# Performance work log

Hardware: AMD Instinct MI355X
Metric: run time of the kernel (lower is better)

The kernel has to match this reference:

```python
import jax, jax.numpy as jnp
import numpy as np

N_HEADS = 32
N_KV_HEADS = 8
HEAD_DIM = 128
DIM = 4096
ROPE_THETA = 500000.0
BSZ, SEQLEN = 4, 1024


def _rope(t, cos, sin):
    # t: [B,S,H,hd]; cos/sin: [S,hd//2]
    te = t[..., 0::2]
    to = t[..., 1::2]
    c = cos[None, :, None, :]
    s = sin[None, :, None, :]
    out = jnp.stack([te * c - to * s, te * s + to * c], axis=-1)
    return out.reshape(t.shape)


def setup_inputs() -> dict:
    key = jax.random.key(0)
    ks = jax.random.split(key, 8)
    scale = 1.0 / np.sqrt(DIM)
    x = jax.random.normal(ks[0], (BSZ, SEQLEN, DIM), dtype=jnp.float32)
    wq = jax.random.normal(ks[1], (DIM, N_HEADS * HEAD_DIM), dtype=jnp.float32) * scale
    wk = jax.random.normal(ks[2], (DIM, N_KV_HEADS * HEAD_DIM), dtype=jnp.float32) * scale
    wv = jax.random.normal(ks[3], (DIM, N_KV_HEADS * HEAD_DIM), dtype=jnp.float32) * scale
    wo = jax.random.normal(ks[4], (N_HEADS * HEAD_DIM, DIM), dtype=jnp.float32) * scale
    # rotary tables: freqs_cis[s, j] = exp(i * s * theta^(-2j/hd))
    inv_freq = 1.0 / (ROPE_THETA ** (np.arange(0, HEAD_DIM, 2, dtype=np.float32) / HEAD_DIM))
    ang = np.outer(np.arange(SEQLEN, dtype=np.float32), inv_freq)
    freqs_cos = jnp.asarray(np.cos(ang), dtype=jnp.float32)
    freqs_sin = jnp.asarray(np.sin(ang), dtype=jnp.float32)
    # additive causal mask: 0 on/below diag, -inf above
    causal_mask = jnp.triu(jnp.full((SEQLEN, SEQLEN), -jnp.inf, dtype=jnp.float32), k=1)
    return {"x": x, "wq": wq, "wk": wk, "wv": wv, "wo": wo,
            "freqs_cos": freqs_cos, "freqs_sin": freqs_sin,
            "causal_mask": causal_mask, "fixed_point_iter": 0, "start_pos": 0}


def reference(x, wq, wk, wv, wo, freqs_cos, freqs_sin, causal_mask, fixed_point_iter, start_pos):
    B, S, _ = x.shape
    n_rep = N_HEADS // N_KV_HEADS
    xq = (x @ wq).reshape(B, S, N_HEADS, HEAD_DIM)
    xk = (x @ wk).reshape(B, S, N_KV_HEADS, HEAD_DIM)
    xv = (x @ wv).reshape(B, S, N_KV_HEADS, HEAD_DIM)
    xq = _rope(xq, freqs_cos, freqs_sin)
    xk = _rope(xk, freqs_cos, freqs_sin)
    # start_pos == 0 prefill: cache slice [:start_pos+S] equals freshly written xk/xv
    keys = jnp.repeat(xk, n_rep, axis=2)    # [B,S,H,hd]
    values = jnp.repeat(xv, n_rep, axis=2)
    scores = jnp.einsum('bqhd,bkhd->bhqk', xq, keys) / np.sqrt(HEAD_DIM)
    scores = scores + causal_mask  # broadcast [S,S]
    probs = jax.nn.softmax(scores.astype(jnp.float32), axis=-1).astype(xq.dtype)
    out = jnp.einsum('bhqk,bkhd->bqhd', probs, values)
    out = out.reshape(B, S, N_HEADS * HEAD_DIM)
    return out @ wo
```

## Files before the change

### kernel.cpp

```cpp
#include <hip/hip_runtime.h>

#define BSZ_  4
#define SEQ_  1024
#define NH_   32
#define NKVH_ 8
#define HD_   128
#define DIM_  4096
#define NTOK_ (BSZ_ * SEQ_)
#define QKVW_ 6144

typedef float  floatx4  __attribute__((ext_vector_type(4)));
typedef float  floatx16 __attribute__((ext_vector_type(16)));
typedef __bf16 bf16x8   __attribute__((ext_vector_type(8)));
typedef unsigned short ushortx8 __attribute__((ext_vector_type(8)));
typedef unsigned int   uint4v   __attribute__((ext_vector_type(4)));

__device__ __forceinline__ float fast_exp2(float x) {
  return __builtin_amdgcn_exp2f(x);
}

__device__ __forceinline__ unsigned short f2bf_bits(float f) {
  unsigned int u = __float_as_uint(f);
  u += 0x7FFFu + ((u >> 16) & 1u);
  return (unsigned short)(u >> 16);
}
__device__ __forceinline__ unsigned int pack_bf2_rne(float lo, float hi_) {
  return (unsigned int)f2bf_bits(lo) | ((unsigned int)f2bf_bits(hi_) << 16);
}
__device__ __forceinline__ unsigned int pack_bf2_trunc(float lo, float hi_) {
  return __builtin_amdgcn_perm(__float_as_uint(hi_), __float_as_uint(lo), 0x07060302u);
}

__device__ __forceinline__ void gld16(const void* g, void* l) {
  __builtin_amdgcn_global_load_lds(
      (const __attribute__((address_space(1))) void*)g,
      (__attribute__((address_space(3))) void*)l, 16, 0, 0);
}

__global__ __launch_bounds__(256)
void xconv(const float* __restrict__ X, unsigned short* __restrict__ XB)
{
  size_t i = ((size_t)blockIdx.x * 256 + threadIdx.x) * 4;
  float4 v = *(const float4*)&X[i];
  ushort4 o;
  o.x = f2bf_bits(v.x); o.y = f2bf_bits(v.y);
  o.z = f2bf_bits(v.z); o.w = f2bf_bits(v.w);
  *(ushort4*)&XB[i] = o;
}

__global__ __launch_bounds__(256)
void wtrans(const float* __restrict__ W, unsigned short* __restrict__ WT,
            int K, int N)
{
  __shared__ unsigned short T[32][36];
  const int k0 = blockIdx.y * 32, n0 = blockIdx.x * 32;
  const int t = threadIdx.x;
  {
    int kr = t >> 3, nc = (t & 7) * 4;
    float4 v = *(const float4*)&W[(size_t)(k0 + kr) * N + n0 + nc];
    T[kr][nc + 0] = f2bf_bits(v.x);
    T[kr][nc + 1] = f2bf_bits(v.y);
    T[kr][nc + 2] = f2bf_bits(v.z);
    T[kr][nc + 3] = f2bf_bits(v.w);
  }
  __syncthreads();
  {
    int nr = t >> 3, kc = (t & 7) * 4;
    ushort4 o;
    o.x = T[kc + 0][nr]; o.y = T[kc + 1][nr];
    o.z = T[kc + 2][nr]; o.w = T[kc + 3][nr];
    *(ushort4*)&WT[(size_t)(n0 + nr) * K + k0 + kc] = o;
  }
}

__global__ __launch_bounds__(256)
void vtrans2(const unsigned short* __restrict__ qkv, unsigned short* __restrict__ VT)
{
  __shared__ unsigned short T[32][36];
  const int bh = blockIdx.z;
  const int s0 = blockIdx.x * 32, d0 = blockIdx.y * 32;
  const int b = bh >> 3, kvh = bh & 7;
  const int t = threadIdx.x;
  {
    int sr = t >> 3, dc = (t & 7) * 4;
    ushort4 v = *(const ushort4*)&qkv[(size_t)(b * SEQ_ + s0 + sr) * QKVW_ + 5120 + kvh * HD_ + d0 + dc];
    T[sr][dc + 0] = v.x; T[sr][dc + 1] = v.y;
    T[sr][dc + 2] = v.z; T[sr][dc + 3] = v.w;
  }
  __syncthreads();
  {
    int dr = t >> 3, sc = (t & 7) * 4;
    ushort4 o;
    o.x = T[sc + 0][dr]; o.y = T[sc + 1][dr];
    o.z = T[sc + 2][dr]; o.w = T[sc + 3][dr];
    *(ushort4*)&VT[((size_t)bh * HD_ + d0 + dr) * SEQ_ + s0 + sc] = o;
  }
}

__global__ __launch_bounds__(256)
void rope2(unsigned int* __restrict__ t, const float* __restrict__ cosf,
           const float* __restrict__ sinf, int shift, int stride_u32, int base_u32)
{
  int idx = blockIdx.x * 256 + threadIdx.x;
  int tok = idx >> shift;
  int rem = idx & ((1 << shift) - 1);
  int d2  = idx & 63;
  int pos = tok & (SEQ_ - 1);
  unsigned int* p = &t[(size_t)tok * stride_u32 + base_u32 + rem];
  unsigned int pv = *p;
  float xe = __uint_as_float(pv << 16);
  float xo = __uint_as_float(pv & 0xFFFF0000u);
  float cv = cosf[pos * 64 + d2];
  float sv = sinf[pos * 64 + d2];
  float oe = xe * cv - xo * sv;
  float oo = xe * sv + xo * cv;
  *p = pack_bf2_rne(oe, oo);
}

template<bool OUT_BF16>
__global__ __launch_bounds__(1024, 4)
void gemm_w16(const unsigned short* __restrict__ A,
              const unsigned short* __restrict__ B,
              void* __restrict__ Cout, int M, int N, int K)
{
  __shared__ __align__(16) unsigned short As[4][256][32];
  __shared__ __align__(16) unsigned short Bs[4][256][32];

  const int tid  = threadIdx.x;
  const int w    = tid >> 6;
  const int lane = tid & 63;
  const int l16  = lane & 15;
  const int quad = lane >> 4;
  const int wr   = w >> 2;
  const int wc   = w & 3;

  int wg = blockIdx.x;
  const int q8 = gridDim.x >> 3;
  wg = (wg & 7) * q8 + (wg >> 3);
  const int nbx = N >> 8;
  const int bm = (wg / nbx) * 256;
  const int bn = (wg % nbx) * 256;

  const int srow = tid >> 2;
  const int scs  = (tid & 3) ^ ((srow >> 1) & 3);
  const unsigned short* Ag = &A[(size_t)(bm + srow) * K + scs * 8];
  const unsigned short* Bg = &B[(size_t)(bn + srow) * K + scs * 8];
  char* AsW = (char*)&As[0][0][0] + w * 1024;
  char* BsW = (char*)&Bs[0][0][0] + w * 1024;

  const int ntiles = K >> 5;

  auto stage = [&](int kt, int buf) {
    size_t ko = (size_t)kt << 5;
    gld16(Ag + ko, AsW + buf * 16384);
    gld16(Bg + ko, BsW + buf * 16384);
  };

  floatx4 acc[4][4];
#pragma unroll
  for (int i = 0; i < 4; i++)
#pragma unroll
    for (int j = 0; j < 4; j++) acc[i][j] = (floatx4){0.f, 0.f, 0.f, 0.f};

  const int cfr = quad ^ ((l16 >> 1) & 3);
  const unsigned short* ArF = &As[0][wr * 64][cfr * 8];
  const unsigned short* BrF = &Bs[0][wc * 64][cfr * 8];

  stage(0, 0); stage(1, 1); stage(2, 2);
  asm volatile("s_waitcnt vmcnt(4)" ::: "memory");
  __builtin_amdgcn_s_barrier();

#pragma unroll 1
  for (int t = 0; t < ntiles; t++) {
    const int buf = t & 3;

    bf16x8 af[4], bfr[4];
    {
      const unsigned short* Ab = ArF + (size_t)buf * (256 * 32) + l16 * 32;
      const unsigned short* Bb = BrF + (size_t)buf * (256 * 32) + l16 * 32;
#pragma unroll
      for (int i = 0; i < 4; i++) af[i]  = *(const bf16x8*)&Ab[i * (16 * 32)];
#pragma unroll
      for (int j = 0; j < 4; j++) bfr[j] = *(const bf16x8*)&Bb[j * (16 * 32)];
    }

    {
      int pk = (t + 3 < ntiles) ? t + 3 : 0;
      stage(pk, (t + 3) & 3);
    }

    __builtin_amdgcn_s_setprio(1);
#pragma unroll
    for (int i = 0; i < 4; i++)
#pragma unroll
      for (int j = 0; j < 4; j++)
        acc[i][j] = __builtin_amdgcn_mfma_f32_16x16x32_bf16(af[i], bfr[j], acc[i][j], 0, 0, 0);
    __builtin_amdgcn_s_setprio(0);

    asm volatile("s_waitcnt vmcnt(4)" ::: "memory");
    __builtin_amdgcn_s_barrier();
  }

  asm volatile("s_waitcnt vmcnt(0)" ::: "memory");

#pragma unroll
  for (int i = 0; i < 4; i++)
#pragma unroll
    for (int j = 0; j < 4; j++)
#pragma unroll
      for (int r = 0; r < 4; r++) {
        size_t row = bm + wr * 64 + i * 16 + quad * 4 + r;
        size_t col = bn + wc * 64 + j * 16 + l16;
        if (OUT_BF16)
          ((unsigned short*)Cout)[row * N + col] = f2bf_bits(acc[i][j][r]);
        else
          ((float*)Cout)[row * N + col] = acc[i][j][r];
      }
}

__global__ __launch_bounds__(256, 2)
void flash_attn2(const unsigned short* __restrict__ qkv,
                 const unsigned short* __restrict__ vt,
                 unsigned short* __restrict__ o)
{
  __shared__ __align__(16) unsigned short S_[4][8192];
  unsigned short* Ks = &S_[0][0];
  unsigned short* Vs = &S_[1][0];

  const int bid = blockIdx.x;
  const int grp = bid >> 7;
  const int idx = bid & 127;
  const int qt = (grp == 0) ? 3 : (grp == 1) ? 2 : (grp == 2) ? 0 : 1;
  const int h = idx & 31, b = idx >> 5;

  const int kvh = h >> 2;
  const int tid = threadIdx.x, w = tid >> 6, lane = tid & 63;
  const int l31 = lane & 31, hi = lane >> 5;
  const int qb = qt * 256, qw = qb + w * 64;

  const float CEXP = (float)(0.08838834764831845 * 1.4426950408889634);

  bf16x8 qf[2][8];
#pragma unroll
  for (int t2 = 0; t2 < 2; t2++) {
    const unsigned short* qrow =
        &qkv[(size_t)(b * SEQ_ + qw + t2 * 32 + l31) * QKVW_ + h * HD_ + hi * 8];
#pragma unroll
    for (int s = 0; s < 8; s++)
      qf[t2][s] = *(const bf16x8*)&qrow[s * 16];
  }

  floatx16 oa[2][4];
#pragma unroll
  for (int t2 = 0; t2 < 2; t2++)
#pragma unroll
    for (int dt = 0; dt < 4; dt++)
#pragma unroll
      for (int r = 0; r < 16; r++) oa[t2][dt][r] = 0.f;

  float ms[2] = {-3.0e38f, -3.0e38f};
  float ls[2] = {0.f, 0.f};

  const int nk = qb + 256;
  const int qmaxw = qw + 63;

  ushortx8 kreg[4], vreg[4];
  const size_t kg0 = (size_t)(b * SEQ_) * QKVW_ + 4096 + kvh * HD_;
  const size_t vg0 = ((size_t)(b * NKVH_ + kvh) * HD_) * SEQ_;
  const int krow = tid >> 4, kc = tid & 15;
  const int vrow = tid >> 3, vc = tid & 7;

  auto issue_loads = [&](int kb) {
    const size_t gb = kg0 + (size_t)kb * QKVW_;
#pragma unroll
    for (int it = 0; it < 4; it++)
      kreg[it] = *(const ushortx8*)&qkv[gb + (size_t)(it * 16 + krow) * QKVW_ + kc * 8];
    const size_t vb = vg0 + kb;
#pragma unroll
    for (int it = 0; it < 4; it++)
      vreg[it] = *(const ushortx8*)&vt[vb + (size_t)(it * 32 + vrow) * SEQ_ + vc * 8];
  };
  auto write_lds = [&]() {
#pragma unroll
    for (int it = 0; it < 4; it++) {
      int key = it * 16 + krow;
      *(ushortx8*)&Ks[key * 128 + ((kc ^ (key & 15)) * 8)] = kreg[it];
    }
#pragma unroll
    for (int it = 0; it < 4; it++) {
      int d = it * 32 + vrow;
      *(ushortx8*)&Vs[d * 64 + ((vc ^ (d & 7)) * 8)] = vreg[it];
    }
  };

  issue_loads(0);

  for (int kb_ = 0; kb_ < nk; kb_ += 64) {
    __syncthreads();
    write_lds();
    if (kb_ + 64 < nk) issue_loads(kb_ + 64);
    asm volatile("s_waitcnt lgkmcnt(0)" ::: "memory");
    __builtin_amdgcn_s_barrier();

    if (kb_ <= qmaxw) {
      const bool needmask = (kb_ + 63 > qw);

#pragma unroll
      for (int t2 = 0; t2 < 2; t2++) {
        floatx16 sc[2];
#pragma unroll
        for (int r = 0; r < 16; r++) { sc[0][r] = 0.f; sc[1][r] = 0.f; }
        __builtin_amdgcn_s_setprio(1);
#pragma unroll
        for (int s = 0; s < 8; s++) {
          int c = 2 * s + hi;
          bf16x8 k0 = *(const bf16x8*)&Ks[l31 * 128 + ((c ^ (l31 & 15)) * 8)];
          bf16x8 k1 = *(const bf16x8*)&Ks[(32 + l31) * 128 + ((c ^ ((32 + l31) & 15)) * 8)];
          sc[0] = __builtin_amdgcn_mfma_f32_32x32x16_bf16(k0, qf[t2][s], sc[0], 0, 0, 0);
          sc[1] = __builtin_amdgcn_mfma_f32_32x32x16_bf16(k1, qf[t2][s], sc[1], 0, 0, 0);
        }
        __builtin_amdgcn_s_setprio(0);

        if (needmask) {
          const int q = qw + t2 * 32 + l31;
#pragma unroll
          for (int k2 = 0; k2 < 2; k2++)
#pragma unroll
            for (int r = 0; r < 16; r++) {
              int key = kb_ + k2 * 32 + (r & 3) + 8 * (r >> 2) + 4 * hi;
              if (key > q) sc[k2][r] = -3.0e38f;
            }
        }

        float mx0 = sc[0][0], mx1 = sc[0][1];
#pragma unroll
        for (int r = 2; r < 16; r += 2) { mx0 = fmaxf(mx0, sc[0][r]); mx1 = fmaxf(mx1, sc[0][r + 1]); }
#pragma unroll
        for (int r = 0; r < 16; r += 2) { mx0 = fmaxf(mx0, sc[1][r]); mx1 = fmaxf(mx1, sc[1][r + 1]); }
        float mx = fmaxf(mx0, mx1);
        mx = fmaxf(mx, __shfl_xor(mx, 32));
        float mxs = mx * CEXP;

        float mn, alpha;
        if (__all(mxs - ms[t2] <= 8.0f)) {
          mn = ms[t2]; alpha = 1.0f;
        } else {
          mn = fmaxf(ms[t2], mxs);
          alpha = fast_exp2(ms[t2] - mn);
          ms[t2] = mn;
        }

        float rs0 = 0.f, rs1 = 0.f;
        unsigned int pk2[2][8];
#pragma unroll
        for (int k2 = 0; k2 < 2; k2++) {
#pragma unroll
          for (int r = 0; r < 16; r += 2) {
            float p0 = fast_exp2(__builtin_fmaf(sc[k2][r],     CEXP, -mn));
            float p1 = fast_exp2(__builtin_fmaf(sc[k2][r + 1], CEXP, -mn));
            rs0 += p0; rs1 += p1;
            pk2[k2][r >> 1] = pack_bf2_trunc(p0, p1);
          }
        }
        float rs = rs0 + rs1;
        rs += __shfl_xor(rs, 32);
        ls[t2] = ls[t2] * alpha + rs;

        if (__any(alpha != 1.0f)) {
#pragma unroll
          for (int dt = 0; dt < 4; dt++)
#pragma unroll
            for (int r = 0; r < 16; r++) oa[t2][dt][r] *= alpha;
        }

        __builtin_amdgcn_s_setprio(1);
#pragma unroll
        for (int ks = 0; ks < 4; ks++) {
          const int k2s = ks >> 1;
          const int sub = (ks & 1) * 4;
          auto w02 = __builtin_amdgcn_permlane32_swap(pk2[k2s][sub + 0], pk2[k2s][sub + 2], false, false);
          auto w13 = __builtin_amdgcn_permlane32_swap(pk2[k2s][sub + 1], pk2[k2s][sub + 3], false, false);
          uint4v pw = (uint4v){(unsigned int)w02[0], (unsigned int)w13[0],
                               (unsigned int)w02[1], (unsigned int)w13[1]};
          bf16x8 pf = __builtin_bit_cast(bf16x8, pw);
          int c = 2 * ks + hi;
#pragma unroll
          for (int dt = 0; dt < 4; dt++) {
            int d = dt * 32 + l31;
            bf16x8 vf = *(const bf16x8*)&Vs[d * 64 + ((c ^ (d & 7)) * 8)];
            oa[t2][dt] = __builtin_amdgcn_mfma_f32_32x32x16_bf16(vf, pf, oa[t2][dt], 0, 0, 0);
          }
        }
        __builtin_amdgcn_s_setprio(0);
      }
    }
  }

  __syncthreads();
  unsigned short* patch = &S_[w][0];
  float inv[2] = {1.0f / ls[0], 1.0f / ls[1]};
#pragma unroll
  for (int t2 = 0; t2 < 2; t2++) {
    const int qloc = t2 * 32 + l31;
#pragma unroll
    for (int dt = 0; dt < 4; dt++)
#pragma unroll
      for (int rq = 0; rq < 4; rq++) {
        float a0 = oa[t2][dt][rq * 4 + 0] * inv[t2];
        float a1 = oa[t2][dt][rq * 4 + 1] * inv[t2];
        float a2 = oa[t2][dt][rq * 4 + 2] * inv[t2];
        float a3 = oa[t2][dt][rq * 4 + 3] * inv[t2];
        int doff = dt * 32 + 8 * rq + 4 * hi;
        int c = doff >> 3;
        uint2 val = {pack_bf2_rne(a0, a1), pack_bf2_rne(a2, a3)};
        *(uint2*)&patch[qloc * 128 + ((c ^ (qloc & 7)) * 8) + (doff & 7)] = val;
      }
  }
#pragma unroll
  for (int it = 0; it < 16; it++) {
    int idx2 = it * 64 + lane;
    int row = idx2 >> 4, c = idx2 & 15;
    int cc = (c & 7) ^ (row & 7);
    int cs = (c & 8) | cc;
    ushortx8 vv = *(const ushortx8*)&patch[row * 128 + cs * 8];
    *(ushortx8*)&o[(size_t)(b * SEQ_ + qb + w * 64 + row) * 4096 + h * HD_ + c * 8] = vv;
  }
}

extern "C" void kernel_launch(void* const* d_in, const int* in_sizes, int n_in,
                              void* d_out, int out_size, void* d_ws, size_t ws_size,
                              hipStream_t stream)
{
  const float* x  = (const float*)d_in[0];
  const float* wq = (const float*)d_in[1];
  const float* wk = (const float*)d_in[2];
  const float* wv = (const float*)d_in[3];
  const float* wo = (const float*)d_in[4];
  const float* fc = (const float*)d_in[5];
  const float* fs = (const float*)d_in[6];
  float* out = (float*)d_out;

  unsigned short* xb    = (unsigned short*)d_ws;
  unsigned short* wqkvT = xb    + (size_t)NTOK_ * DIM_;
  unsigned short* qkvb  = wqkvT + (size_t)QKVW_ * DIM_;
  unsigned short* vtb   = qkvb  + (size_t)NTOK_ * QKVW_;
  unsigned short* ab    = xb;
  unsigned short* woT   = wqkvT;

  dim3 blk(256);

  xconv<<<(NTOK_ * DIM_ / 4) / 256, blk, 0, stream>>>(x, xb);
  wtrans<<<dim3(DIM_ / 32, DIM_ / 32), blk, 0, stream>>>(wq, wqkvT, DIM_, DIM_);
  wtrans<<<dim3((NKVH_ * HD_) / 32, DIM_ / 32), blk, 0, stream>>>(wk, wqkvT + (size_t)4096 * DIM_, DIM_, NKVH_ * HD_);
  wtrans<<<dim3((NKVH_ * HD_) / 32, DIM_ / 32), blk, 0, stream>>>(wv, wqkvT + (size_t)5120 * DIM_, DIM_, NKVH_ * HD_);

  gemm_w16<true><<<dim3((QKVW_ / 256) * (NTOK_ / 256)), dim3(1024), 0, stream>>>(
      xb, wqkvT, qkvb, NTOK_, QKVW_, DIM_);

  wtrans<<<dim3(DIM_ / 32, DIM_ / 32), blk, 0, stream>>>(wo, woT, DIM_, DIM_);

  rope2<<<(NTOK_ * 2048) / 256, blk, 0, stream>>>((unsigned int*)qkvb, fc, fs, 11, 3072, 0);
  rope2<<<(NTOK_ * 512) / 256, blk, 0, stream>>>((unsigned int*)qkvb, fc, fs, 9, 3072, 2048);

  vtrans2<<<dim3(SEQ_ / 32, HD_ / 32, BSZ_ * NKVH_), blk, 0, stream>>>(qkvb, vtb);

  flash_attn2<<<dim3((SEQ_ / 256) * NH_ * BSZ_), blk, 0, stream>>>(qkvb, vtb, ab);

  gemm_w16<false><<<dim3((DIM_ / 256) * (NTOK_ / 256)), dim3(1024), 0, stream>>>(
      ab, woT, out, NTOK_, DIM_, DIM_);
}
```

Measured before the change: 677.8 us.

## Merge weight transposes and rope launches, batch PV MFMAs across query tiles

Combines the three Q/K/V weight-transpose launches into one kernel and the two rope launches into one, cutting launch overhead and tail effects. In flash attention, the P·V MFMA loop is moved out of the per-query-tile loop so each V fragment read from LDS feeds two MFMAs, one per query tile. This halves V LDS reads and interleaves independent MFMA chains. In exchange, the packed probabilities of both tiles stay live at once, which raises register pressure.

```diff
diff --git a/kernel.cpp b/kernel.cpp
--- a/kernel.cpp
+++ b/kernel.cpp
@@ -46,6 +46,36 @@
   o.x = f2bf_bits(v.x); o.y = f2bf_bits(v.y);
   o.z = f2bf_bits(v.z); o.w = f2bf_bits(v.w);
   *(ushort4*)&XB[i] = o;
+}
+
+__global__ __launch_bounds__(256)
+void wtrans3(const float* __restrict__ wq, const float* __restrict__ wk,
+             const float* __restrict__ wv, unsigned short* __restrict__ WT)
+{
+  __shared__ unsigned short T[32][36];
+  const int n0 = blockIdx.x * 32;
+  const int k0 = blockIdx.y * 32;
+  const float* W; int ns0, Nsrc;
+  if (n0 < 4096)      { W = wq; ns0 = n0;        Nsrc = 4096; }
+  else if (n0 < 5120) { W = wk; ns0 = n0 - 4096; Nsrc = 1024; }
+  else                { W = wv; ns0 = n0 - 5120; Nsrc = 1024; }
+  const int t = threadIdx.x;
+  {
+    int kr = t >> 3, nc = (t & 7) * 4;
+    float4 v = *(const float4*)&W[(size_t)(k0 + kr) * Nsrc + ns0 + nc];
+    T[kr][nc + 0] = f2bf_bits(v.x);
+    T[kr][nc + 1] = f2bf_bits(v.y);
+    T[kr][nc + 2] = f2bf_bits(v.z);
+    T[kr][nc + 3] = f2bf_bits(v.w);
+  }
+  __syncthreads();
+  {
+    int nr = t >> 3, kc = (t & 7) * 4;
+    ushort4 o;
+    o.x = T[kc + 0][nr]; o.y = T[kc + 1][nr];
+    o.z = T[kc + 2][nr]; o.w = T[kc + 3][nr];
+    *(ushort4*)&WT[(size_t)(n0 + nr) * DIM_ + k0 + kc] = o;
+  }
 }
 
 __global__ __launch_bounds__(256)
@@ -98,15 +128,17 @@
 }
 
 __global__ __launch_bounds__(256)
-void rope2(unsigned int* __restrict__ t, const float* __restrict__ cosf,
-           const float* __restrict__ sinf, int shift, int stride_u32, int base_u32)
+void rope_all(unsigned int* __restrict__ t, const float* __restrict__ cosf,
+              const float* __restrict__ sinf)
 {
   int idx = blockIdx.x * 256 + threadIdx.x;
-  int tok = idx >> shift;
-  int rem = idx & ((1 << shift) - 1);
-  int d2  = idx & 63;
+  const int NQ = NTOK_ * 2048;
+  int tok, rem, base;
+  if (idx < NQ) { tok = idx >> 11; rem = idx & 2047; base = 0; }
+  else { int j = idx - NQ; tok = j >> 9; rem = j & 511; base = 2048; }
+  int d2  = rem & 63;
   int pos = tok & (SEQ_ - 1);
-  unsigned int* p = &t[(size_t)tok * stride_u32 + base_u32 + rem];
+  unsigned int* p = &t[(size_t)tok * 3072 + base + rem];
   unsigned int pv = *p;
   float xe = __uint_as_float(pv << 16);
   float xo = __uint_as_float(pv & 0xFFFF0000u);
@@ -304,6 +336,7 @@
 
     if (kb_ <= qmaxw) {
       const bool needmask = (kb_ + 63 > qw);
+      unsigned int pkt[2][2][8];
 
 #pragma unroll
       for (int t2 = 0; t2 < 2; t2++) {
@@ -351,7 +384,6 @@
         }
 
         float rs0 = 0.f, rs1 = 0.f;
-        unsigned int pk2[2][8];
 #pragma unroll
         for (int k2 = 0; k2 < 2; k2++) {
 #pragma unroll
@@ -359,7 +391,7 @@
             float p0 = fast_exp2(__builtin_fmaf(sc[k2][r],     CEXP, -mn));
             float p1 = fast_exp2(__builtin_fmaf(sc[k2][r + 1], CEXP, -mn));
             rs0 += p0; rs1 += p1;
-            pk2[k2][r >> 1] = pack_bf2_trunc(p0, p1);
+            pkt[t2][k2][r >> 1] = pack_bf2_trunc(p0, p1);
           }
         }
         float rs = rs0 + rs1;
@@ -372,27 +404,38 @@
 #pragma unroll
             for (int r = 0; r < 16; r++) oa[t2][dt][r] *= alpha;
         }
-
-        __builtin_amdgcn_s_setprio(1);
-#pragma unroll
-        for (int ks = 0; ks < 4; ks++) {
-          const int k2s = ks >> 1;
-          const int sub = (ks & 1) * 4;
-          auto w02 = __builtin_amdgcn_permlane32_swap(pk2[k2s][sub + 0], pk2[k2s][sub + 2], false, false);
-          auto w13 = __builtin_amdgcn_permlane32_swap(pk2[k2s][sub + 1], pk2[k2s][sub + 3], false, false);
+      }
+
+      __builtin_amdgcn_s_setprio(1);
+#pragma unroll
+      for (int ks = 0; ks < 4; ks++) {
+        const int k2s = ks >> 1;
+        const int sub = (ks & 1) * 4;
+        bf16x8 pf0, pf1;
+        {
+          auto w02 = __builtin_amdgcn_permlane32_swap(pkt[0][k2s][sub + 0], pkt[0][k2s][sub + 2], false, false);
+          auto w13 = __builtin_amdgcn_permlane32_swap(pkt[0][k2s][sub + 1], pkt[0][k2s][sub + 3], false, false);
           uint4v pw = (uint4v){(unsigned int)w02[0], (unsigned int)w13[0],
                                (unsigned int)w02[1], (unsigned int)w13[1]};
-          bf16x8 pf = __builtin_bit_cast(bf16x8, pw);
-          int c = 2 * ks + hi;
-#pragma unroll
-          for (int dt = 0; dt < 4; dt++) {
-            int d = dt * 32 + l31;
-            bf16x8 vf = *(const bf16x8*)&Vs[d * 64 + ((c ^ (d & 7)) * 8)];
-            oa[t2][dt] = __builtin_amdgcn_mfma_f32_32x32x16_bf16(vf, pf, oa[t2][dt], 0, 0, 0);
-          }
-        }
-        __builtin_amdgcn_s_setprio(0);
+          pf0 = __builtin_bit_cast(bf16x8, pw);
+        }
+        {
+          auto w02 = __builtin_amdgcn_permlane32_swap(pkt[1][k2s][sub + 0], pkt[1][k2s][sub + 2], false, false);
+          auto w13 = __builtin_amdgcn_permlane32_swap(pkt[1][k2s][sub + 1], pkt[1][k2s][sub + 3], false, false);
+          uint4v pw = (uint4v){(unsigned int)w02[0], (unsigned int)w13[0],
+                               (unsigned int)w02[1], (unsigned int)w13[1]};
+          pf1 = __builtin_bit_cast(bf16x8, pw);
+        }
+        int c = 2 * ks + hi;
+#pragma unroll
+        for (int dt = 0; dt < 4; dt++) {
+          int d = dt * 32 + l31;
+          bf16x8 vf = *(const bf16x8*)&Vs[d * 64 + ((c ^ (d & 7)) * 8)];
+          oa[0][dt] = __builtin_amdgcn_mfma_f32_32x32x16_bf16(vf, pf0, oa[0][dt], 0, 0, 0);
+          oa[1][dt] = __builtin_amdgcn_mfma_f32_32x32x16_bf16(vf, pf1, oa[1][dt], 0, 0, 0);
+        }
       }
+      __builtin_amdgcn_s_setprio(0);
     }
   }
 
@@ -450,17 +493,14 @@
   dim3 blk(256);
 
   xconv<<<(NTOK_ * DIM_ / 4) / 256, blk, 0, stream>>>(x, xb);
-  wtrans<<<dim3(DIM_ / 32, DIM_ / 32), blk, 0, stream>>>(wq, wqkvT, DIM_, DIM_);
-  wtrans<<<dim3((NKVH_ * HD_) / 32, DIM_ / 32), blk, 0, stream>>>(wk, wqkvT + (size_t)4096 * DIM_, DIM_, NKVH_ * HD_);
-  wtrans<<<dim3((NKVH_ * HD_) / 32, DIM_ / 32), blk, 0, stream>>>(wv, wqkvT + (size_t)5120 * DIM_, DIM_, NKVH_ * HD_);
+  wtrans3<<<dim3(QKVW_ / 32, DIM_ / 32), blk, 0, stream>>>(wq, wk, wv, wqkvT);
 
   gemm_w16<true><<<dim3((QKVW_ / 256) * (NTOK_ / 256)), dim3(1024), 0, stream>>>(
       xb, wqkvT, qkvb, NTOK_, QKVW_, DIM_);
 
   wtrans<<<dim3(DIM_ / 32, DIM_ / 32), blk, 0, stream>>>(wo, woT, DIM_, DIM_);
 
-  rope2<<<(NTOK_ * 2048) / 256, blk, 0, stream>>>((unsigned int*)qkvb, fc, fs, 11, 3072, 0);
-  rope2<<<(NTOK_ * 512) / 256, blk, 0, stream>>>((unsigned int*)qkvb, fc, fs, 9, 3072, 2048);
+  rope_all<<<(NTOK_ * 2560) / 256, blk, 0, stream>>>((unsigned int*)qkvb, fc, fs);
 
   vtrans2<<<dim3(SEQ_ / 32, HD_ / 32, BSZ_ * NKVH_), blk, 0, stream>>>(qkvb, vtb);
 
```

Measured after the change: 730.9 us. 7.8% more time.
